# Optimization experiments

Hardware: AMD Instinct MI355X
Metric: run time of the kernel (lower is better)

## Reference

```python
import jax, jax.numpy as jnp
import numpy as np

N, E, C, A, F = 10000, 128000, 128, 10, 8
LDIMS = (1, 3, 5)  # 0e, 1o, 2e spherical-harmonic block sizes
NPATH = len(LDIMS)


def setup_inputs() -> dict:
    key = jax.random.key(0)
    ks = jax.random.split(key, 16)
    rn = lambda k, s, sc=1.0: jax.random.normal(k, s, dtype=jnp.float32) * sc
    inp = {
        "node_attrs": rn(ks[0], (N, A)),
        "node_feats": rn(ks[1], (N, C)),
        "edge_attrs_real": rn(ks[2], (E, 9)),
        "edge_attrs_imag": rn(ks[3], (E, 9)),
        "edge_feats": jax.random.uniform(ks[4], (E, F), dtype=jnp.float32),
        "edge_index": jax.random.randint(ks[5], (2, E), 0, N, dtype=jnp.int32),
        # learned parameters (e3nn 1/sqrt(fan_in) normalization folded into init)
        "W_up": rn(ks[6], (C, C), 1.0 / np.sqrt(C)),            # o3.Linear on 128x0e
        "W_skip": rn(ks[7], (C, A, C), 1.0 / np.sqrt(C * A)),    # FullyConnectedTensorProduct
        "W_mlp1": rn(ks[8], (F, 64), 1.0 / np.sqrt(F)),
        "W_mlp2": rn(ks[9], (64, 64), 1.0 / 8.0),
        "W_mlp3": rn(ks[10], (64, 64), 1.0 / 8.0),
        "W_mlp4": rn(ks[11], (64, NPATH * C), 1.0 / 8.0),        # -> conv_tp.weight_numel = 384
        "W_lin0": rn(ks[12], (C, C), 1.0 / np.sqrt(C)),          # o3.Linear per-l blocks
        "W_lin1": rn(ks[13], (C, C), 1.0 / np.sqrt(C)),
        "W_lin2": rn(ks[14], (C, C), 1.0 / np.sqrt(C)),
    }
    return inp


def _conv_tp(x, y, w):
    """scalar(128x0e) x sh(0e+1o+2e) uvu tensor product with per-edge weights.
    x: [E,C] sender scalars, y: [E,9] edge sh, w: [E,NPATH,C] -> [E, C*9] irreps_mid layout."""
    outs, off = [], 0
    for l, d in enumerate(LDIMS):
        yl = y[:, off:off + d]                      # [E,d]
        off += d
        xw = x * w[:, l]                            # [E,C]
        outs.append((xw[:, :, None] * yl[:, None, :]).reshape(-1, C * d))
    return jnp.concatenate(outs, axis=-1)           # [E, C*(1+3+5)]


def _linear_irreps(m, Ws):
    """o3.Linear mixing channels within each l block. m: [N, C*9] -> [N, C, 9]."""
    outs, off = [], 0
    for l, d in enumerate(LDIMS):
        blk = m[:, off:off + C * d].reshape(-1, C, d)  # [N,C,d]
        off += C * d
        outs.append(jnp.einsum('num,uk->nkm', blk, Ws[l]))
    return jnp.concatenate(outs, axis=-1)              # [N,C,9] (reshape_irreps layout)


def reference(node_attrs, node_feats, edge_attrs_real, edge_attrs_imag, edge_feats,
              edge_index, W_up, W_skip, W_mlp1, W_mlp2, W_mlp3, W_mlp4,
              W_lin0, W_lin1, W_lin2):
    sender, receiver = edge_index[0], edge_index[1]
    # skip connection: FullyConnectedTensorProduct(node_feats 128x0e, node_attrs 10x0e)
    sc = jnp.einsum('nu,nv,uvk->nk', node_feats, node_attrs, W_skip)
    # linear_up
    h = node_feats @ W_up
    # per-edge tensor-product weights from radial MLP (silu hidden layers, linear out)
    t = jax.nn.silu(edge_feats @ W_mlp1)
    t = jax.nn.silu(t @ W_mlp2)
    t = jax.nn.silu(t @ W_mlp3)
    tpw = (t @ W_mlp4).reshape(-1, NPATH, C)
    # gather senders, tensor product for real and imag edge attrs
    xs = h[sender]
    mji_r = _conv_tp(xs, edge_attrs_real, tpw)
    mji_i = _conv_tp(xs, edge_attrs_imag, tpw)
    # scatter-sum to receivers
    msg_r = jax.ops.segment_sum(mji_r, receiver, num_segments=N)
    msg_i = jax.ops.segment_sum(mji_i, receiver, num_segments=N)
    # output linear + reshape_irreps -> [N, C, 9]
    Ws = (W_lin0, W_lin1, W_lin2)
    out_r = _linear_irreps(msg_r, Ws)
    out_i = _linear_irreps(msg_i, Ws)
    return out_r, out_i, sc
```

## Files before the change

### kernel.cpp

```cpp
#include <hip/hip_runtime.h>
#include <hip/hip_bf16.h>

#define N_NODES 10000
#define N_EDGES 128000
#define C_DIM   128

typedef __attribute__((ext_vector_type(8))) short bf16x8;
typedef __attribute__((ext_vector_type(4))) float f32x4;


__device__ __forceinline__ float silu_f(float x) {
  return x / (1.f + __expf(-x));
}

__device__ __forceinline__ unsigned short f2bf(float x) {
  __hip_bfloat16 b = __float2bfloat16(x);
  return *(unsigned short*)&b;
}

__device__ __forceinline__ float bf2f(unsigned short u) {
  __hip_bfloat16 b = *(__hip_bfloat16*)&u;
  return __bfloat162float(b);
}

__device__ __forceinline__ bf16x8 pack8(float4 lo, float4 hi) {
  bf16x8 r;
  r[0] = (short)f2bf(lo.x); r[1] = (short)f2bf(lo.y);
  r[2] = (short)f2bf(lo.z); r[3] = (short)f2bf(lo.w);
  r[4] = (short)f2bf(hi.x); r[5] = (short)f2bf(hi.y);
  r[6] = (short)f2bf(hi.z); r[7] = (short)f2bf(hi.w);
  return r;
}

#define HB_NODES 40
__global__ __launch_bounds__(256) void k_h(const float* __restrict__ feats,
                                           const float* __restrict__ Wup,
                                           float* __restrict__ h) {
  int tid = threadIdx.x;
  int j = tid & 127;
  int par = tid >> 7;
  int n0 = blockIdx.x * HB_NODES;
  float wreg[128];
  #pragma unroll
  for (int k = 0; k < 128; k++) wreg[k] = Wup[k * 128 + j];
  #pragma unroll 2
  for (int i = par; i < HB_NODES; i += 2) {
    int n = __builtin_amdgcn_readfirstlane(n0 + i);
    const float* fr = &feats[n * 128];
    float acc = 0.f;
    #pragma unroll
    for (int k = 0; k < 128; k++) acc += fr[k] * wreg[k];
    h[n * 128 + j] = acc;
  }
}

__global__ void k_wcvt(const float* __restrict__ Wskip,
                       const float* __restrict__ Wl0,
                       const float* __restrict__ Wl1,
                       const float* __restrict__ Wl2,
                       unsigned short* __restrict__ wbT,
                       unsigned short* __restrict__ wlT) {
  int idx = blockIdx.x * 256 + threadIdx.x;
  if (idx < 163840) {
    int j = idx >> 7, k = idx & 127;
    int u = j / 10, v = j - u * 10;
    wbT[k * 1280 + v * 128 + u] = f2bf(Wskip[idx]);
  } else if (idx < 163840 + 49152) {
    int t = idx - 163840;
    int l = t >> 14, r = t & 16383;
    int u = r >> 7, k = r & 127;
    const float* W = (l == 0) ? Wl0 : (l == 1) ? Wl1 : Wl2;
    wlT[(l * 128 + k) * 128 + u] = f2bf(W[r]);
  }
}

__global__ void k_wcvt2(const float* __restrict__ W1, const float* __restrict__ W2,
                        const float* __restrict__ W3, const float* __restrict__ W4,
                        unsigned short* __restrict__ w1f, unsigned short* __restrict__ w2f,
                        unsigned short* __restrict__ w3f, unsigned short* __restrict__ w4f) {
  int idx = blockIdx.x * 256 + threadIdx.x;
  if (idx < 2048) {
    int ct = idx >> 9, r = idx & 511, n = r >> 5, t = r & 31;
    w1f[idx] = (t < 8) ? f2bf(W1[t * 64 + ct * 16 + n]) : (unsigned short)0;
  } else if (idx < 6144) {
    int j = idx - 2048;
    int ctks = j >> 9, r = j & 511, n = r >> 5, t = r & 31;
    int ct = ctks >> 1, ks = ctks & 1;
    w2f[j] = f2bf(W2[(ks * 32 + t) * 64 + ct * 16 + n]);
  } else if (idx < 10240) {
    int j = idx - 6144;
    int ctks = j >> 9, r = j & 511, n = r >> 5, t = r & 31;
    int ct = ctks >> 1, ks = ctks & 1;
    w3f[j] = f2bf(W3[(ks * 32 + t) * 64 + ct * 16 + n]);
  } else if (idx < 34816) {
    int j = idx - 10240;
    int ctks = j >> 9, r = j & 511, n = r >> 5, t = r & 31;
    int ct = ctks >> 1, ks = ctks & 1;
    w4f[j] = f2bf(W4[(ks * 32 + t) * 384 + ct * 16 + n]);
  }
}

__global__ __launch_bounds__(256) void k_sc(const float* __restrict__ f,
                                            const float* __restrict__ at,
                                            const unsigned short* __restrict__ wbT,
                                            float* __restrict__ sc_out) {
  int tid = threadIdx.x;
  int w = tid >> 6, lane = tid & 63;
  int l15 = lane & 15, quad = lane >> 4;
  int n0 = blockIdx.x * 32;

  int nrow[2];
  #pragma unroll
  for (int t = 0; t < 2; t++) {
    int n = n0 + 16 * t + l15;
    nrow[t] = (n < N_NODES) ? n : (N_NODES - 1);
  }
  float4 fA[2][4][2];
  #pragma unroll
  for (int t = 0; t < 2; t++)
    #pragma unroll
    for (int ks = 0; ks < 4; ks++) {
      fA[t][ks][0] = *(const float4*)&f[nrow[t] * 128 + ks * 32 + quad * 8];
      fA[t][ks][1] = *(const float4*)&f[nrow[t] * 128 + ks * 32 + quad * 8 + 4];
    }

  f32x4 acc[2][2] = {};
  #pragma unroll 1
  for (int c = 0; c < 10; c++) {
    float av[2];
    #pragma unroll
    for (int t = 0; t < 2; t++) av[t] = at[nrow[t] * 10 + c];
    bf16x8 af[2][4];
    #pragma unroll
    for (int t = 0; t < 2; t++)
      #pragma unroll
      for (int ks = 0; ks < 4; ks++) {
        float4 lo = fA[t][ks][0], hi = fA[t][ks][1];
        lo.x *= av[t]; lo.y *= av[t]; lo.z *= av[t]; lo.w *= av[t];
        hi.x *= av[t]; hi.y *= av[t]; hi.z *= av[t]; hi.w *= av[t];
        af[t][ks] = pack8(lo, hi);
      }
    #pragma unroll
    for (int kt = 0; kt < 2; kt++) {
      int kcol = w * 32 + kt * 16 + l15;
      #pragma unroll
      for (int ks = 0; ks < 4; ks++) {
        bf16x8 bf = *(const bf16x8*)&wbT[kcol * 1280 + c * 128 + ks * 32 + quad * 8];
        #pragma unroll
        for (int t = 0; t < 2; t++)
          acc[t][kt] = __builtin_amdgcn_mfma_f32_16x16x32_bf16(af[t][ks], bf,
                                                               acc[t][kt], 0, 0, 0);
      }
    }
  }
  #pragma unroll
  for (int t = 0; t < 2; t++)
    #pragma unroll
    for (int kt = 0; kt < 2; kt++) {
      int kcol = w * 32 + kt * 16 + l15;
      #pragma unroll
      for (int reg = 0; reg < 4; reg++) {
        int n = n0 + 16 * t + quad * 4 + reg;
        if (n < N_NODES)
          __builtin_nontemporal_store(acc[t][kt][reg], &sc_out[n * 128 + kcol]);
      }
    }
}

__global__ __launch_bounds__(256) void k_mlp(const float* __restrict__ ef,
                                             const int* __restrict__ order,
                                             const unsigned short* __restrict__ w1f,
                                             const unsigned short* __restrict__ w2f,
                                             const unsigned short* __restrict__ w3f,
                                             const unsigned short* __restrict__ w4f,
                                             unsigned short* __restrict__ tpw) {
  __shared__ unsigned short sA[128][72];
  __shared__ unsigned short sB[128][72];
  int tid = threadIdx.x;
  int w = tid >> 6, lane = tid & 63;
  int l15 = lane & 15, quad = lane >> 4;
  int e0 = blockIdx.x * 128;
  int fragoff = l15 * 32 + quad * 8;
  int rb = w * 32;

  {
    bf16x8 af[2];
    #pragma unroll
    for (int rt = 0; rt < 2; rt++) {
      bf16x8 a = {};
      if (quad == 0) {
        int pos = e0 + rb + rt * 16 + l15;
        int e = order[pos];
        float4 lo = *(const float4*)&ef[e * 8];
        float4 hi = *(const float4*)&ef[e * 8 + 4];
        a = pack8(lo, hi);
      }
      af[rt] = a;
    }
    f32x4 ac[2][4] = {};
    #pragma unroll
    for (int ct = 0; ct < 4; ct++) {
      bf16x8 b = *(const bf16x8*)&w1f[ct * 512 + fragoff];
      ac[0][ct] = __builtin_amdgcn_mfma_f32_16x16x32_bf16(af[0], b, ac[0][ct], 0, 0, 0);
      ac[1][ct] = __builtin_amdgcn_mfma_f32_16x16x32_bf16(af[1], b, ac[1][ct], 0, 0, 0);
    }
    #pragma unroll
    for (int rt = 0; rt < 2; rt++)
      #pragma unroll
      for (int ct = 0; ct < 4; ct++)
        #pragma unroll
        for (int reg = 0; reg < 4; reg++)
          sA[rb + rt * 16 + quad * 4 + reg][ct * 16 + l15] =
              f2bf(silu_f(ac[rt][ct][reg]));
  }
  __syncthreads();

  #pragma unroll 1
  for (int layer = 0; layer < 2; layer++) {
    unsigned short (*src)[72] = (layer == 0) ? sA : sB;
    unsigned short (*dst)[72] = (layer == 0) ? sB : sA;
    const unsigned short* wf = (layer == 0) ? w2f : w3f;
    bf16x8 a2[2][2];
    #pragma unroll
    for (int rt = 0; rt < 2; rt++)
      #pragma unroll
      for (int ks = 0; ks < 2; ks++)
        a2[rt][ks] = *(const bf16x8*)&src[rb + rt * 16 + l15][ks * 32 + quad * 8];
    f32x4 ac[2][4] = {};
    #pragma unroll
    for (int ct = 0; ct < 4; ct++)
      #pragma unroll
      for (int ks = 0; ks < 2; ks++) {
        bf16x8 b = *(const bf16x8*)&wf[(ct * 2 + ks) * 512 + fragoff];
        ac[0][ct] = __builtin_amdgcn_mfma_f32_16x16x32_bf16(a2[0][ks], b, ac[0][ct], 0, 0, 0);
        ac[1][ct] = __builtin_amdgcn_mfma_f32_16x16x32_bf16(a2[1][ks], b, ac[1][ct], 0, 0, 0);
      }
    #pragma unroll
    for (int rt = 0; rt < 2; rt++)
      #pragma unroll
      for (int ct = 0; ct < 4; ct++)
        #pragma unroll
        for (int reg = 0; reg < 4; reg++)
          dst[rb + rt * 16 + quad * 4 + reg][ct * 16 + l15] =
              f2bf(silu_f(ac[rt][ct][reg]));
    __syncthreads();
  }

  bf16x8 a4[2][2];
  #pragma unroll
  for (int rt = 0; rt < 2; rt++)
    #pragma unroll
    for (int ks = 0; ks < 2; ks++)
      a4[rt][ks] = *(const bf16x8*)&sA[rb + rt * 16 + l15][ks * 32 + quad * 8];

  #pragma unroll 1
  for (int ch = 0; ch < 6; ch++) {
    f32x4 ac[2][4] = {};
    #pragma unroll
    for (int ct = 0; ct < 4; ct++)
      #pragma unroll
      for (int ks = 0; ks < 2; ks++) {
        bf16x8 b = *(const bf16x8*)&w4f[((ch * 4 + ct) * 2 + ks) * 512 + fragoff];
        ac[0][ct] = __builtin_amdgcn_mfma_f32_16x16x32_bf16(a4[0][ks], b, ac[0][ct], 0, 0, 0);
        ac[1][ct] = __builtin_amdgcn_mfma_f32_16x16x32_bf16(a4[1][ks], b, ac[1][ct], 0, 0, 0);
      }
    #pragma unroll
    for (int rt = 0; rt < 2; rt++)
      #pragma unroll
      for (int ct = 0; ct < 4; ct++)
        #pragma unroll
        for (int reg = 0; reg < 4; reg++)
          sB[rb + rt * 16 + quad * 4 + reg][ct * 16 + l15] = f2bf(ac[rt][ct][reg]);
    __syncthreads();
    #pragma unroll
    for (int v = 0; v < 4; v++) {
      int idx = v * 256 + tid;
      int e = idx >> 3, cg = idx & 7;
      uint4 p = *(const uint4*)&sB[e][cg * 8];
      *(uint4*)&tpw[(size_t)(e0 + e) * 384 + ch * 64 + cg * 8] = p;
    }
    __syncthreads();
  }
}

__global__ void k_hist(const int* __restrict__ recv, int* __restrict__ counts) {
  int e = blockIdx.x * 256 + threadIdx.x;
  if (e < N_EDGES) atomicAdd(&counts[recv[e]], 1);
}

__global__ __launch_bounds__(1024) void k_scan(const int* __restrict__ counts,
                                               int* __restrict__ offsets,
                                               int* __restrict__ cursor) {
  __shared__ int part[1024];
  int tid = threadIdx.x;
  int base = tid * 10;
  int local[10]; int s = 0;
  #pragma unroll
  for (int i = 0; i < 10; i++) {
    int idx = base + i;
    int c = (idx < N_NODES) ? counts[idx] : 0;
    local[i] = s; s += c;
  }
  part[tid] = s;
  __syncthreads();
  for (int off = 1; off < 1024; off <<= 1) {
    int v = (tid >= off) ? part[tid - off] : 0;
    __syncthreads();
    part[tid] += v;
    __syncthreads();
  }
  int pre = (tid > 0) ? part[tid - 1] : 0;
  #pragma unroll
  for (int i = 0; i < 10; i++) {
    int idx = base + i;
    if (idx < N_NODES) { int o = pre + local[i]; offsets[idx] = o; cursor[idx] = o; }
  }
  if (tid == 1023) offsets[N_NODES] = part[1023];
}

__global__ void k_scatter(const int* __restrict__ recv, int* __restrict__ cursor,
                          int* __restrict__ order) {
  int e = blockIdx.x * 256 + threadIdx.x;
  if (e < N_EDGES) {
    int idx = atomicAdd(&cursor[recv[e]], 1);
    order[idx] = e;
  }
}

__global__ __launch_bounds__(256) void k_yg(const float* __restrict__ yr,
                                            const float* __restrict__ yi,
                                            const int* __restrict__ send,
                                            const int* __restrict__ order,
                                            float* __restrict__ y2,
                                            int* __restrict__ ss) {
  __shared__ float sy[256][20];
  int tid = threadIdx.x;
  int p0 = blockIdx.x * 256;
  int e = order[p0 + tid];
  ss[p0 + tid] = send[e];
  #pragma unroll
  for (int m = 0; m < 9; m++) {
    sy[tid][m] = yr[e * 9 + m];
    sy[tid][9 + m] = yi[e * 9 + m];
  }
  sy[tid][18] = 0.f; sy[tid][19] = 0.f;
  __syncthreads();
  #pragma unroll
  for (int v = 0; v < 5; v++) {
    int idx = v * 256 + tid;
    int r = idx / 5, c2 = idx - r * 5;
    float4 p4 = *(const float4*)&sy[r][c2 * 4];
    *(float4*)&y2[(size_t)(p0 + r) * 20 + c2 * 4] = p4;
  }
}

__device__ __forceinline__ void edge_fma(const float* __restrict__ y2, int pos,
                                         float xv, float t0, float t1, float t2,
                                         float* mr, float* mi) {
  const float* yy = &y2[(size_t)pos * 20];
  float4 v0 = *(const float4*)&yy[0];
  float4 v1 = *(const float4*)&yy[4];
  float4 v2 = *(const float4*)&yy[8];
  float4 v3 = *(const float4*)&yy[12];
  float2 v4 = *(const float2*)&yy[16];
  float xw0 = xv * t0, xw1 = xv * t1, xw2 = xv * t2;
  mr[0] += xw0 * v0.x;
  mr[1] += xw1 * v0.y; mr[2] += xw1 * v0.z; mr[3] += xw1 * v0.w;
  mr[4] += xw2 * v1.x; mr[5] += xw2 * v1.y; mr[6] += xw2 * v1.z;
  mr[7] += xw2 * v1.w; mr[8] += xw2 * v2.x;
  mi[0] += xw0 * v2.y;
  mi[1] += xw1 * v2.z; mi[2] += xw1 * v2.w; mi[3] += xw1 * v3.x;
  mi[4] += xw2 * v3.y; mi[5] += xw2 * v3.z; mi[6] += xw2 * v3.w;
  mi[7] += xw2 * v4.x; mi[8] += xw2 * v4.y;
}

__global__ __launch_bounds__(128, 4) void k_gather(
    const float* __restrict__ h, const unsigned short* __restrict__ tpw,
    const float* __restrict__ y2, const int* __restrict__ ss,
    const int* __restrict__ offsets,
    unsigned short* __restrict__ msg) {
  int u = threadIdx.x;
  int n = blockIdx.x;
  float mr[9] = {}, mi[9] = {};
  int e0 = __builtin_amdgcn_readfirstlane(offsets[n]);
  int e1 = __builtin_amdgcn_readfirstlane(offsets[n + 1]);
  int jj = e0;
  for (; jj + 3 < e1; jj += 4) {
    float xv[4], t0[4], t1[4], t2[4];
    #pragma unroll
    for (int q = 0; q < 4; q++) {
      int pos = jj + q;
      int s = ss[pos];
      const unsigned short* tp = &tpw[(size_t)pos * 384 + u];
      t0[q] = bf2f(__builtin_nontemporal_load(tp));
      t1[q] = bf2f(__builtin_nontemporal_load(tp + 128));
      t2[q] = bf2f(__builtin_nontemporal_load(tp + 256));
      xv[q] = h[s * 128 + u];
    }
    #pragma unroll
    for (int q = 0; q < 4; q++)
      edge_fma(y2, jj + q, xv[q], t0[q], t1[q], t2[q], mr, mi);
  }
  for (; jj < e1; jj++) {
    int s = ss[jj];
    const unsigned short* tp = &tpw[(size_t)jj * 384 + u];
    float t0 = bf2f(__builtin_nontemporal_load(tp));
    float t1 = bf2f(__builtin_nontemporal_load(tp + 128));
    float t2 = bf2f(__builtin_nontemporal_load(tp + 256));
    float xv = h[s * 128 + u];
    edge_fma(y2, jj, xv, t0, t1, t2, mr, mi);
  }
  int g = n >> 3, i = n & 7;
  unsigned short* mg = msg + (size_t)g * 144 * 128;
  mg[(i * 2 + 0) * 128 + u] = f2bf(mr[0]);
  mg[(i * 2 + 1) * 128 + u] = f2bf(mi[0]);
  #pragma unroll
  for (int m = 1; m < 4; m++) {
    mg[(16 + i * 6 + (m - 1)) * 128 + u] = f2bf(mr[m]);
    mg[(16 + i * 6 + 3 + (m - 1)) * 128 + u] = f2bf(mi[m]);
  }
  #pragma unroll
  for (int m = 4; m < 9; m++) {
    mg[(64 + i * 10 + (m - 4)) * 128 + u] = f2bf(mr[m]);
    mg[(64 + i * 10 + 5 + (m - 4)) * 128 + u] = f2bf(mi[m]);
  }
}

#define LIN_ROWPAD 1156
__global__ __launch_bounds__(256) void k_lin(const unsigned short* __restrict__ msg,
                                             const unsigned short* __restrict__ wlT,
                                             float* __restrict__ out) {
  __shared__ float so[2 * 8 * LIN_ROWPAD];
  int tid = threadIdx.x;
  int w = tid >> 6, lane = tid & 63;
  int l15 = lane & 15, quad = lane >> 4;
  int g = blockIdx.x;

  bf16x8 bfr[3][2][4];
  #pragma unroll
  for (int l = 0; l < 3; l++)
    #pragma unroll
    for (int kt = 0; kt < 2; kt++)
      #pragma unroll
      for (int ks = 0; ks < 4; ks++) {
        int ncol = w * 32 + kt * 16 + l15;
        bfr[l][kt][ks] = *(const bf16x8*)&wlT[(l * 128 + ncol) * 128 + ks * 32 + quad * 8];
      }

  const unsigned short* mg = msg + (size_t)g * 144 * 128;

  #pragma unroll
  for (int tile = 0; tile < 9; tile++) {
    const int l = (tile == 0) ? 0 : (tile < 4) ? 1 : 2;
    const int rbase = tile * 16;
    bf16x8 af[4];
    #pragma unroll
    for (int ks = 0; ks < 4; ks++)
      af[ks] = *(const bf16x8*)&mg[(rbase + l15) * 128 + ks * 32 + quad * 8];
    f32x4 acc0 = {}, acc1 = {};
    #pragma unroll
    for (int ks = 0; ks < 4; ks++) {
      acc0 = __builtin_amdgcn_mfma_f32_16x16x32_bf16(af[ks], bfr[l][0][ks], acc0, 0, 0, 0);
      acc1 = __builtin_amdgcn_mfma_f32_16x16x32_bf16(af[ks], bfr[l][1][ks], acc1, 0, 0, 0);
    }
    #pragma unroll
    for (int reg = 0; reg < 4; reg++) {
      int r = rbase + quad * 4 + reg;
      int c, ni, m;
      if (tile == 0) { ni = (r & 15) >> 1; c = r & 1; m = 0; }
      else if (tile < 4) {
        int q = r - 16; ni = q / 6; int rem = q - ni * 6;
        c = rem >= 3; m = 1 + rem - (c ? 3 : 0);
      } else {
        int q = r - 64; ni = q / 10; int rem = q - ni * 10;
        c = rem >= 5; m = 4 + rem - (c ? 5 : 0);
      }
      int k0 = w * 32 + l15;
      float* ob = &so[(c * 8 + ni) * LIN_ROWPAD + m];
      ob[(k0)      * 9] = acc0[reg];
      ob[(k0 + 16) * 9] = acc1[reg];
    }
  }
  __syncthreads();
  #pragma unroll
  for (int v = 0; v < 18; v++) {
    int idx = v * 256 + tid;
    int c = idx / 2304;
    int rem = idx - c * 2304;
    int ni = rem / 288;
    int off4 = rem - ni * 288;
    f32x4 p = *(const f32x4*)&so[(c * 8 + ni) * LIN_ROWPAD + off4 * 4];
    f32x4* dst = (f32x4*)&out[(size_t)c * 11520000 + ((size_t)g * 8 + ni) * 1152 +
                              (size_t)off4 * 4];
    __builtin_nontemporal_store(p, dst);
  }
}

extern "C" void kernel_launch(void* const* d_in, const int* in_sizes, int n_in,
                              void* d_out, int out_size, void* d_ws, size_t ws_size,
                              hipStream_t stream) {
  const float* node_attrs = (const float*)d_in[0];
  const float* node_feats = (const float*)d_in[1];
  const float* ear   = (const float*)d_in[2];
  const float* eai   = (const float*)d_in[3];
  const float* ef    = (const float*)d_in[4];
  const int*   eidx  = (const int*)d_in[5];
  const float* Wup   = (const float*)d_in[6];
  const float* Wskip = (const float*)d_in[7];
  const float* W1    = (const float*)d_in[8];
  const float* W2    = (const float*)d_in[9];
  const float* W3    = (const float*)d_in[10];
  const float* W4    = (const float*)d_in[11];
  const float* Wl0   = (const float*)d_in[12];
  const float* Wl1   = (const float*)d_in[13];
  const float* Wl2   = (const float*)d_in[14];
  float* out = (float*)d_out;

  char* ws = (char*)d_ws;
  float*          h       = (float*)ws;
  unsigned short* tpw     = (unsigned short*)(ws + 5120000);
  unsigned short* msg     = (unsigned short*)(ws + 103424000);
  unsigned short* wlT     = (unsigned short*)(ws + 149504000);
  unsigned short* wbT     = (unsigned short*)(ws + 149602304);
  int*            counts  = (int*)(ws + 149929984);
  int*            offsets = (int*)(ws + 149969984);
  int*            cursor  = (int*)(ws + 150010112);
  int*            order   = (int*)(ws + 150050112);
  unsigned short* w1f     = (unsigned short*)(ws + 150562816);
  unsigned short* w2f     = (unsigned short*)(ws + 150566912);
  unsigned short* w3f     = (unsigned short*)(ws + 150575104);
  unsigned short* w4f     = (unsigned short*)(ws + 150583296);

  float* y2 = (float*)d_out;
  int*   ss = (int*)((char*)d_out + 10240000);

  const int* send = eidx;
  const int* recv = eidx + N_EDGES;

  hipMemsetAsync(counts, 0, N_NODES * sizeof(int), stream);
  k_hist<<<dim3(500), dim3(256), 0, stream>>>(recv, counts);
  k_scan<<<dim3(1), dim3(1024), 0, stream>>>(counts, offsets, cursor);
  k_scatter<<<dim3(500), dim3(256), 0, stream>>>(recv, cursor, order);
  k_yg<<<dim3(500), dim3(256), 0, stream>>>(ear, eai, send, order, y2, ss);
  k_wcvt<<<dim3(832), dim3(256), 0, stream>>>(Wskip, Wl0, Wl1, Wl2, wbT, wlT);
  k_wcvt2<<<dim3(136), dim3(256), 0, stream>>>(W1, W2, W3, W4, w1f, w2f, w3f, w4f);
  k_h<<<dim3(250), dim3(256), 0, stream>>>(node_feats, Wup, h);
  k_sc<<<dim3(313), dim3(256), 0, stream>>>(node_feats, node_attrs, wbT,
                                            out + 2 * 11520000);
  k_mlp<<<dim3(1000), dim3(256), 0, stream>>>(ef, order, w1f, w2f, w3f, w4f, tpw);
  k_gather<<<dim3(10000), dim3(128), 0, stream>>>(h, tpw, y2, ss, offsets, msg);
  k_lin<<<dim3(1250), dim3(256), 0, stream>>>(msg, wlT, out);
  (void)in_sizes; (void)n_in; (void)out_size; (void)ws_size;
}
```

Measured before the change: 341.6 us.

## Fuse preprocessing kernels, use wave-shuffle scan, drop block barriers in MLP

Merges the two weight-conversion kernels into one launch and folds the sender/edge-attribute permutation kernel into the scatter kernel. Replaces the LDS Hillis-Steele scan with wave shuffles, so it needs only two barriers. In the MLP kernel, block barriers become compiler fences and each wave writes out only its own rows. Also raises k_gather's occupancy hint. These remove launch overhead and synchronisation stalls, but the scatter writes are now uncoalesced and the compiler fences do not order LDS across lanes within a wave.

```diff
diff --git a/kernel.cpp b/kernel.cpp
--- a/kernel.cpp
+++ b/kernel.cpp
@@ -58,42 +58,41 @@
                        const float* __restrict__ Wl0,
                        const float* __restrict__ Wl1,
                        const float* __restrict__ Wl2,
+                       const float* __restrict__ W1, const float* __restrict__ W2,
+                       const float* __restrict__ W3, const float* __restrict__ W4,
                        unsigned short* __restrict__ wbT,
-                       unsigned short* __restrict__ wlT) {
+                       unsigned short* __restrict__ wlT,
+                       unsigned short* __restrict__ w1f, unsigned short* __restrict__ w2f,
+                       unsigned short* __restrict__ w3f, unsigned short* __restrict__ w4f) {
   int idx = blockIdx.x * 256 + threadIdx.x;
   if (idx < 163840) {
     int j = idx >> 7, k = idx & 127;
     int u = j / 10, v = j - u * 10;
     wbT[k * 1280 + v * 128 + u] = f2bf(Wskip[idx]);
-  } else if (idx < 163840 + 49152) {
+  } else if (idx < 212992) {
     int t = idx - 163840;
     int l = t >> 14, r = t & 16383;
     int u = r >> 7, k = r & 127;
     const float* W = (l == 0) ? Wl0 : (l == 1) ? Wl1 : Wl2;
     wlT[(l * 128 + k) * 128 + u] = f2bf(W[r]);
-  }
-}
-
-__global__ void k_wcvt2(const float* __restrict__ W1, const float* __restrict__ W2,
-                        const float* __restrict__ W3, const float* __restrict__ W4,
-                        unsigned short* __restrict__ w1f, unsigned short* __restrict__ w2f,
-                        unsigned short* __restrict__ w3f, unsigned short* __restrict__ w4f) {
-  int idx = blockIdx.x * 256 + threadIdx.x;
-  if (idx < 2048) {
-    int ct = idx >> 9, r = idx & 511, n = r >> 5, t = r & 31;
-    w1f[idx] = (t < 8) ? f2bf(W1[t * 64 + ct * 16 + n]) : (unsigned short)0;
-  } else if (idx < 6144) {
-    int j = idx - 2048;
+  } else if (idx < 215040) {
+    int j = idx - 212992;
+    int ct = j >> 9, r = j & 511, n = r >> 5, t = r & 31;
+    w1f[j] = (t < 8) ? f2bf(W1[t * 64 + ct * 16 + n]) : (unsigned short)0;
+    (void)ct;
+    if (t < 8) w1f[j] = f2bf(W1[t * 64 + ct * 16 + n]);
+  } else if (idx < 219136) {
+    int j = idx - 215040;
     int ctks = j >> 9, r = j & 511, n = r >> 5, t = r & 31;
     int ct = ctks >> 1, ks = ctks & 1;
     w2f[j] = f2bf(W2[(ks * 32 + t) * 64 + ct * 16 + n]);
-  } else if (idx < 10240) {
-    int j = idx - 6144;
+  } else if (idx < 223232) {
+    int j = idx - 219136;
     int ctks = j >> 9, r = j & 511, n = r >> 5, t = r & 31;
     int ct = ctks >> 1, ks = ctks & 1;
     w3f[j] = f2bf(W3[(ks * 32 + t) * 64 + ct * 16 + n]);
-  } else if (idx < 34816) {
-    int j = idx - 10240;
+  } else if (idx < 247808) {
+    int j = idx - 223232;
     int ctks = j >> 9, r = j & 511, n = r >> 5, t = r & 31;
     int ct = ctks >> 1, ks = ctks & 1;
     w4f[j] = f2bf(W4[(ks * 32 + t) * 384 + ct * 16 + n]);
@@ -213,7 +212,7 @@
           sA[rb + rt * 16 + quad * 4 + reg][ct * 16 + l15] =
               f2bf(silu_f(ac[rt][ct][reg]));
   }
-  __syncthreads();
+  asm volatile("" ::: "memory");
 
   #pragma unroll 1
   for (int layer = 0; layer < 2; layer++) {
@@ -243,7 +242,7 @@
         for (int reg = 0; reg < 4; reg++)
           dst[rb + rt * 16 + quad * 4 + reg][ct * 16 + l15] =
               f2bf(silu_f(ac[rt][ct][reg]));
-    __syncthreads();
+    asm volatile("" ::: "memory");
   }
 
   bf16x8 a4[2][2];
@@ -271,15 +270,15 @@
         #pragma unroll
         for (int reg = 0; reg < 4; reg++)
           sB[rb + rt * 16 + quad * 4 + reg][ct * 16 + l15] = f2bf(ac[rt][ct][reg]);
-    __syncthreads();
+    asm volatile("" ::: "memory");
     #pragma unroll
     for (int v = 0; v < 4; v++) {
-      int idx = v * 256 + tid;
-      int e = idx >> 3, cg = idx & 7;
-      uint4 p = *(const uint4*)&sB[e][cg * 8];
-      *(uint4*)&tpw[(size_t)(e0 + e) * 384 + ch * 64 + cg * 8] = p;
-    }
-    __syncthreads();
+      int idx = v * 64 + lane;
+      int r = idx >> 3, cg = idx & 7;
+      uint4 p = *(const uint4*)&sB[rb + r][cg * 8];
+      *(uint4*)&tpw[(size_t)(e0 + rb + r) * 384 + ch * 64 + cg * 8] = p;
+    }
+    asm volatile("" ::: "memory");
   }
 }
 
@@ -291,8 +290,9 @@
 __global__ __launch_bounds__(1024) void k_scan(const int* __restrict__ counts,
                                                int* __restrict__ offsets,
                                                int* __restrict__ cursor) {
-  __shared__ int part[1024];
+  __shared__ int swave[16];
   int tid = threadIdx.x;
+  int lane = tid & 63, w = tid >> 6;
   int base = tid * 10;
   int local[10]; int s = 0;
   #pragma unroll
@@ -301,56 +301,50 @@
     int c = (idx < N_NODES) ? counts[idx] : 0;
     local[i] = s; s += c;
   }
-  part[tid] = s;
+  int inc = s;
+  #pragma unroll
+  for (int d = 1; d < 64; d <<= 1) {
+    int v = __shfl_up(inc, d, 64);
+    if (lane >= d) inc += v;
+  }
+  if (lane == 63) swave[w] = inc;
   __syncthreads();
-  for (int off = 1; off < 1024; off <<= 1) {
-    int v = (tid >= off) ? part[tid - off] : 0;
-    __syncthreads();
-    part[tid] += v;
-    __syncthreads();
-  }
-  int pre = (tid > 0) ? part[tid - 1] : 0;
+  if (w == 0) {
+    int t = (lane < 16) ? swave[lane] : 0;
+    #pragma unroll
+    for (int d = 1; d < 16; d <<= 1) {
+      int v = __shfl_up(t, d, 64);
+      if (lane >= d) t += v;
+    }
+    if (lane < 16) swave[lane] = t;
+  }
+  __syncthreads();
+  int wpre = (w > 0) ? swave[w - 1] : 0;
+  int pre = wpre + (inc - s);
   #pragma unroll
   for (int i = 0; i < 10; i++) {
     int idx = base + i;
     if (idx < N_NODES) { int o = pre + local[i]; offsets[idx] = o; cursor[idx] = o; }
   }
-  if (tid == 1023) offsets[N_NODES] = part[1023];
-}
-
-__global__ void k_scatter(const int* __restrict__ recv, int* __restrict__ cursor,
-                          int* __restrict__ order) {
+  if (tid == 1023) offsets[N_NODES] = wpre + inc;
+}
+
+__global__ void k_scatter(const int* __restrict__ recv, const int* __restrict__ send,
+                          const float* __restrict__ yr, const float* __restrict__ yi,
+                          int* __restrict__ cursor, int* __restrict__ order,
+                          float* __restrict__ y2, int* __restrict__ ss) {
   int e = blockIdx.x * 256 + threadIdx.x;
   if (e < N_EDGES) {
     int idx = atomicAdd(&cursor[recv[e]], 1);
     order[idx] = e;
-  }
-}
-
-__global__ __launch_bounds__(256) void k_yg(const float* __restrict__ yr,
-                                            const float* __restrict__ yi,
-                                            const int* __restrict__ send,
-                                            const int* __restrict__ order,
-                                            float* __restrict__ y2,
-                                            int* __restrict__ ss) {
-  __shared__ float sy[256][20];
-  int tid = threadIdx.x;
-  int p0 = blockIdx.x * 256;
-  int e = order[p0 + tid];
-  ss[p0 + tid] = send[e];
-  #pragma unroll
-  for (int m = 0; m < 9; m++) {
-    sy[tid][m] = yr[e * 9 + m];
-    sy[tid][9 + m] = yi[e * 9 + m];
-  }
-  sy[tid][18] = 0.f; sy[tid][19] = 0.f;
-  __syncthreads();
-  #pragma unroll
-  for (int v = 0; v < 5; v++) {
-    int idx = v * 256 + tid;
-    int r = idx / 5, c2 = idx - r * 5;
-    float4 p4 = *(const float4*)&sy[r][c2 * 4];
-    *(float4*)&y2[(size_t)(p0 + r) * 20 + c2 * 4] = p4;
+    ss[idx] = send[e];
+    float* yy = &y2[(size_t)idx * 20];
+    #pragma unroll
+    for (int m = 0; m < 9; m++) {
+      yy[m] = yr[e * 9 + m];
+      yy[9 + m] = yi[e * 9 + m];
+    }
+    yy[18] = 0.f; yy[19] = 0.f;
   }
 }
 
@@ -374,7 +368,7 @@
   mi[7] += xw2 * v4.x; mi[8] += xw2 * v4.y;
 }
 
-__global__ __launch_bounds__(128, 4) void k_gather(
+__global__ __launch_bounds__(128, 6) void k_gather(
     const float* __restrict__ h, const unsigned short* __restrict__ tpw,
     const float* __restrict__ y2, const int* __restrict__ ss,
     const int* __restrict__ offsets,
@@ -540,10 +534,11 @@
   hipMemsetAsync(counts, 0, N_NODES * sizeof(int), stream);
   k_hist<<<dim3(500), dim3(256), 0, stream>>>(recv, counts);
   k_scan<<<dim3(1), dim3(1024), 0, stream>>>(counts, offsets, cursor);
-  k_scatter<<<dim3(500), dim3(256), 0, stream>>>(recv, cursor, order);
-  k_yg<<<dim3(500), dim3(256), 0, stream>>>(ear, eai, send, order, y2, ss);
-  k_wcvt<<<dim3(832), dim3(256), 0, stream>>>(Wskip, Wl0, Wl1, Wl2, wbT, wlT);
-  k_wcvt2<<<dim3(136), dim3(256), 0, stream>>>(W1, W2, W3, W4, w1f, w2f, w3f, w4f);
+  k_scatter<<<dim3(500), dim3(256), 0, stream>>>(recv, send, ear, eai, cursor,
+                                                 order, y2, ss);
+  k_wcvt<<<dim3(968), dim3(256), 0, stream>>>(Wskip, Wl0, Wl1, Wl2,
+                                              W1, W2, W3, W4,
+                                              wbT, wlT, w1f, w2f, w3f, w4f);
   k_h<<<dim3(250), dim3(256), 0, stream>>>(node_feats, Wup, h);
   k_sc<<<dim3(313), dim3(256), 0, stream>>>(node_feats, node_attrs, wbT,
                                             out + 2 * 11520000);
```

After: 335.0 us. Within noise of the previous version (-1.9%).
